# Optimization experiments

Hardware: AMD Instinct MI355X
Metric: run time of the kernel (lower is better)

## Reference

```python
import jax, jax.numpy as jnp
import numpy as np


def setup_inputs() -> dict:
    key = jax.random.key(0)
    k1, k2, k3 = jax.random.split(key, 3)
    B, S, H, D = 4, 4096, 16, 128
    C, K = H * D, 4
    return {
        "hidden_states": jax.random.normal(k1, (B, S, H, D), dtype=jnp.float32),
        "conv_weight": jax.random.normal(k2, (C, K), dtype=jnp.float32) * 0.1,
        "conv_bias": jax.random.normal(k3, (C,), dtype=jnp.float32) * 0.1,
    }


def reference(hidden_states, conv_weight, conv_bias):
    # hidden_states: [B, S, H, D] -> [B, C, S] with C = H*D
    B, S, H, D = hidden_states.shape
    C = H * D
    K = conv_weight.shape[-1]
    x = hidden_states.reshape(B, S, C).transpose(0, 2, 1)  # [B, C, S]
    # Depthwise causal conv1d: left-pad K-1, groups=C
    y = jax.lax.conv_general_dilated(
        x,
        conv_weight[:, None, :],  # [C, 1, K]
        window_strides=(1,),
        padding=[(K - 1, 0)],
        dimension_numbers=("NCH", "OIH", "NCH"),
        feature_group_count=C,
    )  # [B, C, S]
    y = jax.nn.silu(y + conv_bias[None, :, None])
    # reshape(bsz, n_heads, head_dim, seq_len).transpose(-1, -2)
    return y.reshape(B, H, D, S).transpose(0, 1, 3, 2)  # [B, H, S, D]
```

## Files before the change

### kernel.cpp

```cpp
#include <hip/hip_runtime.h>


constexpr int Bb = 4, Ss = 4096, Hh = 16, Dd = 128, Cc = 2048, Kk = 4;
constexpr int SEQ  = 8;
constexpr int CPB  = 1024;
constexpr int TPB  = 8;
constexpr int RING = 20;
constexpr int STRIPS = Ss / (SEQ * TPB);

union F4 {
    float4 v;
    float f[4];
};

__device__ __forceinline__ void gload1k(const float* g, float* l) {
    __builtin_amdgcn_global_load_lds(
        (const __attribute__((address_space(1))) void*)g,
        (__attribute__((address_space(3))) void*)l,
        16, 0, 0);
}

__global__ __launch_bounds__(256, 2) void titans_conv(
    const float* __restrict__ x,
    const float* __restrict__ w,
    const float* __restrict__ bias,
    float* __restrict__ out)
{
    __shared__ float lds[RING * CPB];

    const int t     = threadIdx.x;
    const int wv    = t >> 6;
    const int ln    = t & 63;
    const int strip = (int)blockIdx.x;
    const int b     = (int)blockIdx.y;
    const int cb    = (int)blockIdx.z * CPB;
    const int c0    = cb + t * 4;
    const int S0    = strip * (SEQ * TPB);

    const float* xb = x + (size_t)b * Ss * Cc + cb;

    float wf[4][4], bv[4];
    {
        const float4* wp = (const float4*)(w + (size_t)c0 * Kk);
        F4 u0, u1, u2, u3, ub;
        u0.v = wp[0]; u1.v = wp[1]; u2.v = wp[2]; u3.v = wp[3];
        ub.v = *(const float4*)(bias + c0);
        #pragma unroll
        for (int k = 0; k < 4; ++k) {
            wf[0][k] = u0.f[k]; wf[1][k] = u1.f[k];
            wf[2][k] = u2.f[k]; wf[3][k] = u3.f[k];
        }
        #pragma unroll
        for (int j = 0; j < 4; ++j) bv[j] = ub.f[j];
    }

    if (strip > 0) {
        #pragma unroll
        for (int k = 0; k < 11; ++k) {
            const int sidx = wv * 11 + k;
            const int lr = sidx >> 2, q = sidx & 3;
            gload1k(xb + (size_t)(S0 - 3 + lr) * Cc + q * 256 + ln * 4,
                    &lds[lr * CPB + q * 256]);
        }
    } else {
        #pragma unroll
        for (int r = 0; r < 3; ++r)
            *(float4*)&lds[r * CPB + t * 4] = float4{0.f, 0.f, 0.f, 0.f};
        #pragma unroll
        for (int k = 0; k < 8; ++k) {
            const int sidx = wv * 8 + k;
            const int lr = 3 + (sidx >> 2), q = sidx & 3;
            gload1k(xb + (size_t)(S0 - 3 + lr) * Cc + q * 256 + ln * 4,
                    &lds[lr * CPB + q * 256]);
        }
    }
    __syncthreads();

    const int h = c0 >> 7;
    const int d = c0 & 127;
    float* orow = out + (((size_t)b * Hh + h) * Ss + S0) * Dd + d;

    #pragma unroll
    for (int tt = 0; tt < TPB; ++tt) {
        if (tt + 1 < TPB) {
            const int base = (8 * tt + 11) % RING;
            #pragma unroll
            for (int k = 0; k < 8; ++k) {
                const int rr = wv * 2 + (k >> 2);
                const int q  = k & 3;
                int sl = base + rr;
                if (sl >= RING) sl -= RING;
                gload1k(xb + (size_t)(S0 + 8 + 8 * tt + rr) * Cc + q * 256 + ln * 4,
                        &lds[sl * CPB + q * 256]);
            }
        }

        F4 rows[SEQ + 3];
        #pragma unroll
        for (int i = 0; i < SEQ + 3; ++i) {
            const int sl = (8 * tt + i) % RING;
            rows[i].v = *(const float4*)&lds[sl * CPB + t * 4];
        }
        #pragma unroll
        for (int i = 0; i < SEQ; ++i) {
            F4 res;
            #pragma unroll
            for (int j = 0; j < 4; ++j) {
                float z = bv[j];
                z = fmaf(wf[j][0], rows[i + 0].f[j], z);
                z = fmaf(wf[j][1], rows[i + 1].f[j], z);
                z = fmaf(wf[j][2], rows[i + 2].f[j], z);
                z = fmaf(wf[j][3], rows[i + 3].f[j], z);
                float e = __expf(-z);
                res.f[j] = z * __builtin_amdgcn_rcpf(1.0f + e);
            }
            *(float4*)(orow + (size_t)(tt * SEQ + i) * Dd) = res.v;
        }

        __syncthreads();
    }
}

extern "C" void kernel_launch(void* const* d_in, const int* in_sizes, int n_in,
                              void* d_out, int out_size, void* d_ws, size_t ws_size,
                              hipStream_t stream) {
    const float* x    = (const float*)d_in[0];
    const float* w    = (const float*)d_in[1];
    const float* bias = (const float*)d_in[2];
    float* out        = (float*)d_out;

    dim3 grid(STRIPS, Bb, Cc / CPB);
    titans_conv<<<grid, 256, 0, stream>>>(x, w, bias, out);
}
```

Before: 240.0 us.

## Make each wave load its own LDS columns and drop block barriers

```diff
diff --git a/kernel.cpp b/kernel.cpp
--- a/kernel.cpp
+++ b/kernel.cpp
@@ -8,9 +8,12 @@
 constexpr int RING = 20;
 constexpr int STRIPS = Ss / (SEQ * TPB);
 
+typedef float nf4 __attribute__((ext_vector_type(4)));
+
 union F4 {
     float4 v;
-    float f[4];
+    nf4    n;
+    float  f[4];
 };
 
 __device__ __forceinline__ void gload1k(const float* g, float* l) {
@@ -20,7 +23,7 @@
         16, 0, 0);
 }
 
-__global__ __launch_bounds__(256, 2) void titans_conv(
+__global__ __launch_bounds__(256, 4) void titans_conv(
     const float* __restrict__ x,
     const float* __restrict__ w,
     const float* __restrict__ bias,
@@ -37,7 +40,8 @@
     const int c0    = cb + t * 4;
     const int S0    = strip * (SEQ * TPB);
 
-    const float* xb = x + (size_t)b * Ss * Cc + cb;
+    const float* xw = x + (size_t)b * Ss * Cc + cb + wv * 256 + ln * 4;
+    float* lw = &lds[wv * 256];
 
     float wf[4][4], bv[4];
     {
@@ -56,25 +60,16 @@
 
     if (strip > 0) {
         #pragma unroll
-        for (int k = 0; k < 11; ++k) {
-            const int sidx = wv * 11 + k;
-            const int lr = sidx >> 2, q = sidx & 3;
-            gload1k(xb + (size_t)(S0 - 3 + lr) * Cc + q * 256 + ln * 4,
-                    &lds[lr * CPB + q * 256]);
-        }
+        for (int r = 0; r < 11; ++r)
+            gload1k(xw + (size_t)(S0 - 3 + r) * Cc, lw + r * CPB);
     } else {
         #pragma unroll
         for (int r = 0; r < 3; ++r)
             *(float4*)&lds[r * CPB + t * 4] = float4{0.f, 0.f, 0.f, 0.f};
         #pragma unroll
-        for (int k = 0; k < 8; ++k) {
-            const int sidx = wv * 8 + k;
-            const int lr = 3 + (sidx >> 2), q = sidx & 3;
-            gload1k(xb + (size_t)(S0 - 3 + lr) * Cc + q * 256 + ln * 4,
-                    &lds[lr * CPB + q * 256]);
-        }
+        for (int r = 3; r < 11; ++r)
+            gload1k(xw + (size_t)(S0 - 3 + r) * Cc, lw + r * CPB);
     }
-    __syncthreads();
 
     const int h = c0 >> 7;
     const int d = c0 & 127;
@@ -82,18 +77,8 @@
 
     #pragma unroll
     for (int tt = 0; tt < TPB; ++tt) {
-        if (tt + 1 < TPB) {
-            const int base = (8 * tt + 11) % RING;
-            #pragma unroll
-            for (int k = 0; k < 8; ++k) {
-                const int rr = wv * 2 + (k >> 2);
-                const int q  = k & 3;
-                int sl = base + rr;
-                if (sl >= RING) sl -= RING;
-                gload1k(xb + (size_t)(S0 + 8 + 8 * tt + rr) * Cc + q * 256 + ln * 4,
-                        &lds[sl * CPB + q * 256]);
-            }
-        }
+        if (tt == 0) asm volatile("s_waitcnt vmcnt(0)" ::: "memory");
+        else         asm volatile("s_waitcnt vmcnt(8)" ::: "memory");
 
         F4 rows[SEQ + 3];
         #pragma unroll
@@ -101,6 +86,17 @@
             const int sl = (8 * tt + i) % RING;
             rows[i].v = *(const float4*)&lds[sl * CPB + t * 4];
         }
+
+        if (tt + 1 < TPB) {
+            #pragma unroll
+            for (int r = 0; r < 8; ++r) {
+                const int ar = 8 * tt + 11 + r;
+                gload1k(xw + (size_t)(S0 - 3 + ar) * Cc,
+                        lw + (ar % RING) * CPB);
+            }
+        }
+        __builtin_amdgcn_sched_barrier(0);
+
         #pragma unroll
         for (int i = 0; i < SEQ; ++i) {
             F4 res;
@@ -114,10 +110,9 @@
                 float e = __expf(-z);
                 res.f[j] = z * __builtin_amdgcn_rcpf(1.0f + e);
             }
-            *(float4*)(orow + (size_t)(tt * SEQ + i) * Dd) = res.v;
+            __builtin_nontemporal_store(res.n,
+                (nf4*)(orow + (size_t)(tt * SEQ + i) * Dd));
         }
-
-        __syncthreads();
     }
 }
 
```

Result: no change. 241.0 us (+0.4%).
